# Performance work log

Measured on AMD Instinct MI355X. Metric: run time of the kernel, lower is better.

## Reference

```python
import jax, jax.numpy as jnp
import numpy as np

DIM_Q = 512
DIM_K = 512
DIM_V = 512
NUM_HEADS = 8
B, NQ, NK = 4, 2048, 2048


def _linear_init(key, d_in, d_out):
    kw, kb = jax.random.split(key)
    bound = 1.0 / np.sqrt(d_in)
    W = jax.random.uniform(kw, (d_in, d_out), minval=-bound, maxval=bound, dtype=jnp.float32)
    b = jax.random.uniform(kb, (d_out,), minval=-bound, maxval=bound, dtype=jnp.float32)
    return W, b


def setup_inputs() -> dict:
    key = jax.random.key(0)
    ks = jax.random.split(key, 6)
    Q = jax.random.normal(ks[0], (B, NQ, DIM_Q), dtype=jnp.float32)
    K = jax.random.normal(ks[1], (B, NK, DIM_K), dtype=jnp.float32)
    Wq, bq = _linear_init(ks[2], DIM_Q, DIM_V)
    Wk, bk = _linear_init(ks[3], DIM_K, DIM_V)
    Wv, bv = _linear_init(ks[4], DIM_K, DIM_V)
    Wo, bo = _linear_init(ks[5], DIM_V, DIM_V)
    ln0_g = jnp.ones((DIM_V,), jnp.float32)
    ln0_b = jnp.zeros((DIM_V,), jnp.float32)
    ln1_g = jnp.ones((DIM_V,), jnp.float32)
    ln1_b = jnp.zeros((DIM_V,), jnp.float32)
    return {"Q": Q, "K": K, "Wq": Wq, "bq": bq, "Wk": Wk, "bk": bk,
            "Wv": Wv, "bv": bv, "Wo": Wo, "bo": bo,
            "ln0_g": ln0_g, "ln0_b": ln0_b, "ln1_g": ln1_g, "ln1_b": ln1_b}


def _layer_norm(x, g, b, eps=1e-5):
    mu = jnp.mean(x, axis=-1, keepdims=True)
    var = jnp.mean(jnp.square(x - mu), axis=-1, keepdims=True)
    return (x - mu) * jax.lax.rsqrt(var + eps) * g + b


def reference(Q, K, Wq, bq, Wk, bk, Wv, bv, Wo, bo, ln0_g, ln0_b, ln1_g, ln1_b):
    h = NUM_HEADS
    dh = DIM_V // h
    q = Q @ Wq + bq                      # [B, NQ, DIM_V]
    k = K @ Wk + bk                      # [B, NK, DIM_V]
    v = K @ Wv + bv                      # [B, NK, DIM_V]
    qh = q.reshape(B, NQ, h, dh)
    kh = k.reshape(B, NK, h, dh)
    vh = v.reshape(B, NK, h, dh)
    # NOTE: faithful to original — scale by sqrt(dim_V), not sqrt(head_dim)
    scores = jnp.einsum('bqhd,bkhd->bhqk', qh, kh) / jnp.sqrt(jnp.float32(DIM_V))
    A = jax.nn.softmax(scores, axis=-1)  # [B, h, NQ, NK]
    o = jnp.einsum('bhqk,bkhd->bqhd', A, vh) + qh
    H = o.reshape(B, NQ, DIM_V)          # residual with projected Q
    H = _layer_norm(H, ln0_g, ln0_b)
    H = H + jax.nn.relu(H @ Wo + bo)
    H = _layer_norm(H, ln1_g, ln1_b)
    return H
```

## Files before the change

### kernel.cpp

```cpp
#include <hip/hip_runtime.h>

typedef float f32x4 __attribute__((ext_vector_type(4)));
typedef float f32x16 __attribute__((ext_vector_type(16)));
typedef __bf16 bf16x8 __attribute__((ext_vector_type(8)));
typedef unsigned short u16;
typedef u16 u16x8 __attribute__((ext_vector_type(8)));
typedef u16 u16x4 __attribute__((ext_vector_type(4)));

#define SCALE2F (0.044194173824159216f * 1.4426950408889634f)
#define UNSCALE (1.0f / SCALE2F)

__device__ __forceinline__ u16 f2bf(float x){ return __builtin_bit_cast(u16, (__bf16)x); }
__device__ __forceinline__ float bf2f(u16 h){ unsigned u = ((unsigned)h) << 16; return __builtin_bit_cast(float, u); }
__device__ __forceinline__ int swz(int r, int byteInRow){ return (r*128 + byteInRow) ^ ((r & 7) << 4); }
__device__ __forceinline__ void gload16(const void* g, void* l) {
  __builtin_amdgcn_global_load_lds(
      (const __attribute__((address_space(1))) void*)g,
      (__attribute__((address_space(3))) void*)l, 16, 0, 0);
}

#define MFMA(a,b,c)   __builtin_amdgcn_mfma_f32_16x16x32_bf16((a),(b),(c),0,0,0)
#define MFMA32(a,b,c) __builtin_amdgcn_mfma_f32_32x32x16_bf16((a),(b),(c),0,0,0)

__global__ __launch_bounds__(256) void wprep_k(
    const float* __restrict__ W0, const float* __restrict__ W1,
    const float* __restrict__ W2, const float* __restrict__ W3,
    u16* __restrict__ wt)
{
  __shared__ float tile[64][68];
  const float* Ws[4] = {W0, W1, W2, W3};
  const float* W = Ws[blockIdx.z];
  const float sc = (blockIdx.z == 0) ? SCALE2F : 1.0f;
  u16* out = wt + (size_t)blockIdx.z * 512 * 512;
  int k0 = blockIdx.x * 64, n0 = blockIdx.y * 64;
  int t = threadIdx.x;
  #pragma unroll
  for (int i = 0; i < 2; ++i) {
    int c = t + i*256; int r = c >> 3, k8 = c & 7;
    const float* src = W + (size_t)(k0 + r)*512 + n0 + k8*8;
    *(f32x4*)&tile[r][k8*8]     = *(const f32x4*)src;
    *(f32x4*)&tile[r][k8*8 + 4] = *(const f32x4*)(src + 4);
  }
  __syncthreads();
  #pragma unroll
  for (int i = 0; i < 2; ++i) {
    int c = t + i*256; int r = c >> 3, k8 = c & 7;
    u16x8 h;
    #pragma unroll
    for (int j = 0; j < 8; ++j) h[j] = f2bf(tile[k8*8 + j][r] * sc);
    *(u16x8*)(out + (size_t)(n0 + r)*512 + k0 + k8*8) = h;
  }
}

__global__ __launch_bounds__(512) void proj3_k(
    const float* __restrict__ Qin, const float* __restrict__ Kin,
    const u16* __restrict__ wt,
    const float* __restrict__ bq, const float* __restrict__ bk, const float* __restrict__ bv,
    u16* __restrict__ qbuf, u16* __restrict__ kbuf, u16* __restrict__ vt)
{
  __shared__ __align__(16) u16 lA[2][64*64];
  __shared__ __align__(16) u16 lB[2][128*64];
  int z = blockIdx.z;
  const float* A    = (z == 0) ? Qin : Kin;
  const u16*   Bt   = wt + (size_t)z * 262144;
  const float* bias = (z == 0) ? bq : (z == 1) ? bk : bv;
  const float bscale = (z == 0) ? SCALE2F : 1.0f;
  int row0 = blockIdx.x * 64, col0 = blockIdx.y * 128;
  int t = threadIdx.x, lane = t & 63, wid = t >> 6;
  int wr = wid >> 2, wc = wid & 3;
  int l15 = lane & 15, lg = lane >> 4;
  int ar = t >> 3, ak8 = t & 7;
  int br = t >> 3;
  int bsrc = (((t & 7) << 4) ^ ((br & 7) << 4)) >> 1;
  const float* Arow = A + (size_t)row0 * 512;
  const u16*   Brow = Bt + (size_t)col0 * 512;

  f32x4 acc[2][2] = {};

  #pragma unroll
  for (int i = 0; i < 2; ++i)
    gload16(Brow + (size_t)(br + i*64)*512 + bsrc, (char*)lB[0] + i*8192 + t*16);
  {
    const float* src = Arow + (size_t)ar*512 + ak8*8;
    f32x4 x0 = *(const f32x4*)src;
    f32x4 x1 = *(const f32x4*)(src + 4);
    u16x8 h;
    #pragma unroll
    for (int j = 0; j < 4; ++j) { h[j] = f2bf(x0[j]); h[j+4] = f2bf(x1[j]); }
    *(u16x8*)((char*)lA[0] + swz(ar, ak8*16)) = h;
  }
  __syncthreads();

  int cur = 0;
  for (int k0 = 0; k0 < 512; k0 += 64) {
    bool pf = (k0 + 64 < 512);
    f32x4 px0, px1;
    if (pf) {
      #pragma unroll
      for (int i = 0; i < 2; ++i)
        gload16(Brow + (size_t)(br + i*64)*512 + k0 + 64 + bsrc, (char*)lB[cur^1] + i*8192 + t*16);
      const float* src = Arow + (size_t)ar*512 + k0 + 64 + ak8*8;
      px0 = *(const f32x4*)src;
      px1 = *(const f32x4*)(src + 4);
    }
    const char* lAc = (const char*)lA[cur];
    const char* lBc = (const char*)lB[cur];
    #pragma unroll
    for (int ks = 0; ks < 2; ++ks) {
      bf16x8 af[2], bfv[2];
      #pragma unroll
      for (int m = 0; m < 2; ++m)
        af[m] = *(const bf16x8*)(lAc + swz(wr*32 + m*16 + l15, ks*64 + lg*16));
      #pragma unroll
      for (int n = 0; n < 2; ++n)
        bfv[n] = *(const bf16x8*)(lBc + swz(wc*32 + n*16 + l15, ks*64 + lg*16));
      #pragma unroll
      for (int m = 0; m < 2; ++m)
        #pragma unroll
        for (int n = 0; n < 2; ++n)
          acc[m][n] = MFMA(af[m], bfv[n], acc[m][n]);
    }
    if (pf) {
      u16x8 h;
      #pragma unroll
      for (int j = 0; j < 4; ++j) { h[j] = f2bf(px0[j]); h[j+4] = f2bf(px1[j]); }
      *(u16x8*)((char*)lA[cur^1] + swz(ar, ak8*16)) = h;
    }
    __syncthreads();
    cur ^= 1;
  }

  if (z < 2) {
    u16* out = z ? kbuf : qbuf;
    #pragma unroll
    for (int m = 0; m < 2; ++m) {
      int rowg = row0 + wr*32 + m*16 + lg*4;
      #pragma unroll
      for (int n = 0; n < 2; ++n) {
        int colg = col0 + wc*32 + n*16 + l15;
        float bvv = bias[colg] * bscale;
        #pragma unroll
        for (int r = 0; r < 4; ++r)
          out[(size_t)(rowg + r)*512 + colg] = f2bf(acc[m][n][r] + bvv);
      }
    }
  } else {
    #pragma unroll
    for (int m = 0; m < 2; ++m) {
      int rowg = row0 + wr*32 + m*16 + lg*4;
      int b = rowg >> 11, ntok = rowg & 2047;
      #pragma unroll
      for (int n = 0; n < 2; ++n) {
        int colg = col0 + wc*32 + n*16 + l15;
        float bvv = bias[colg];
        u16x4 hv;
        #pragma unroll
        for (int r = 0; r < 4; ++r) hv[r] = f2bf(acc[m][n][r] + bvv);
        *(u16x4*)(vt + ((size_t)b*512 + colg)*2048 + ntok) = hv;
      }
    }
  }
}

__global__ __launch_bounds__(512) void gemmo_k(
    const u16* __restrict__ A, const u16* __restrict__ Bt,
    const float* __restrict__ bias, float* __restrict__ outf,
    const u16* __restrict__ resid)
{
  __shared__ __align__(16) u16 lA[2][64*64];
  __shared__ __align__(16) u16 lB[2][128*64];
  int row0 = blockIdx.x * 64, col0 = blockIdx.y * 128;
  int t = threadIdx.x, lane = t & 63, wid = t >> 6;
  int wr = wid >> 2, wc = wid & 3;
  int l15 = lane & 15, lg = lane >> 4;
  int ar = t >> 3;
  int asrc = (((t & 7) << 4) ^ ((ar & 7) << 4)) >> 1;
  const u16* Arow = A + (size_t)row0 * 512;
  const u16* Brow = Bt + (size_t)col0 * 512;
  f32x4 acc[2][2] = {};

  gload16(Arow + (size_t)ar*512 + asrc, (char*)lA[0] + t*16);
  #pragma unroll
  for (int i = 0; i < 2; ++i)
    gload16(Brow + (size_t)(ar + i*64)*512 + asrc, (char*)lB[0] + i*8192 + t*16);
  __syncthreads();

  int cur = 0;
  for (int k0 = 0; k0 < 512; k0 += 64) {
    if (k0 + 64 < 512) {
      gload16(Arow + (size_t)ar*512 + k0 + 64 + asrc, (char*)lA[cur^1] + t*16);
      #pragma unroll
      for (int i = 0; i < 2; ++i)
        gload16(Brow + (size_t)(ar + i*64)*512 + k0 + 64 + asrc, (char*)lB[cur^1] + i*8192 + t*16);
    }
    const char* lAc = (const char*)lA[cur];
    const char* lBc = (const char*)lB[cur];
    #pragma unroll
    for (int ks = 0; ks < 2; ++ks) {
      bf16x8 af[2], bfv[2];
      #pragma unroll
      for (int m = 0; m < 2; ++m)
        af[m] = *(const bf16x8*)(lAc + swz(wr*32 + m*16 + l15, ks*64 + lg*16));
      #pragma unroll
      for (int n = 0; n < 2; ++n)
        bfv[n] = *(const bf16x8*)(lBc + swz(wc*32 + n*16 + l15, ks*64 + lg*16));
      #pragma unroll
      for (int m = 0; m < 2; ++m)
        #pragma unroll
        for (int n = 0; n < 2; ++n)
          acc[m][n] = MFMA(af[m], bfv[n], acc[m][n]);
    }
    __syncthreads();
    cur ^= 1;
  }
  #pragma unroll
  for (int m = 0; m < 2; ++m) {
    int rowg = row0 + wr*32 + m*16 + lg*4;
    #pragma unroll
    for (int n = 0; n < 2; ++n) {
      int colg = col0 + wc*32 + n*16 + l15;
      float bvv = bias[colg];
      #pragma unroll
      for (int r = 0; r < 4; ++r) {
        size_t idx = (size_t)(rowg + r)*512 + colg;
        outf[idx] = bf2f(resid[idx]) + fmaxf(acc[m][n][r] + bvv, 0.0f);
      }
    }
  }
}

__global__ __launch_bounds__(512, 4) void attn_k(
    const u16* __restrict__ qb, const u16* __restrict__ kb,
    const u16* __restrict__ vt, float* __restrict__ opart, float* __restrict__ psb)
{
  __shared__ __align__(16) u16 lK[2][64*64];
  __shared__ __align__(16) u16 lV[2][64*64];
  __shared__ __align__(16) u16 pl[8][32][72];

  int t = threadIdx.x, lane = t & 63, wid = t >> 6;
  int bh = blockIdx.y;
  int b = bh >> 3, h = bh & 7;
  int zkv = blockIdx.z;
  int kvbeg = zkv * 1024, kvend = kvbeg + 1024;
  int q0 = blockIdx.x * 256 + wid * 32;
  int l31 = lane & 31, hi = lane >> 5;

  const u16* kbase = kb + ((size_t)b*2048)*512 + h*64;
  const u16* vbase = vt + ((size_t)b*512 + h*64)*2048;

  int sr = t >> 3;
  int ssrc = (((t & 7) << 4) ^ ((sr & 7) << 4)) >> 1;

  bf16x8 aq[4];
  {
    const u16* qp = qb + ((size_t)(b*2048 + q0 + l31))*512 + h*64 + hi*8;
    #pragma unroll
    for (int ks = 0; ks < 4; ++ks) aq[ks] = *(const bf16x8*)(qp + ks*16);
  }

  f32x16 acco[2] = {};
  float ps = 0.0f;

  gload16(kbase + (size_t)(kvbeg + sr)*512 + ssrc, (char*)lK[0] + t*16);
  gload16(vbase + (size_t)sr*2048 + kvbeg + ssrc, (char*)lV[0] + t*16);
  __syncthreads();

  int cur = 0;
  for (int t0 = kvbeg; t0 < kvend; t0 += 64) {
    if (t0 + 64 < kvend) {
      gload16(kbase + (size_t)(t0 + 64 + sr)*512 + ssrc, (char*)lK[cur^1] + t*16);
      gload16(vbase + (size_t)sr*2048 + t0 + 64 + ssrc, (char*)lV[cur^1] + t*16);
    }
    const char* lKc = (const char*)lK[cur];
    const char* lVc = (const char*)lV[cur];
    #pragma unroll
    for (int n = 0; n < 2; ++n) {
      f32x16 s = {};
      #pragma unroll
      for (int ks = 0; ks < 4; ++ks) {
        bf16x8 kf = *(const bf16x8*)(lKc + swz(n*32 + l31, ks*32 + hi*16));
        s = MFMA32(kf, aq[ks], s);
      }
      #pragma unroll
      for (int rq = 0; rq < 4; ++rq) {
        u16x4 hp;
        #pragma unroll
        for (int e = 0; e < 4; ++e) {
          float p = __builtin_amdgcn_exp2f(s[rq*4 + e]);
          ps += p;
          hp[e] = f2bf(p);
        }
        *(u16x4*)&pl[wid][l31][n*32 + rq*8 + hi*4] = hp;
      }
    }
    bf16x8 pf[4];
    #pragma unroll
    for (int ks = 0; ks < 4; ++ks)
      pf[ks] = *(const bf16x8*)&pl[wid][l31][ks*16 + hi*8];
    #pragma unroll
    for (int m = 0; m < 2; ++m)
      #pragma unroll
      for (int ks = 0; ks < 4; ++ks) {
        bf16x8 vf = *(const bf16x8*)(lVc + swz(m*32 + l31, ks*32 + hi*16));
        acco[m] = MFMA32(vf, pf[ks], acco[m]);
      }
    __syncthreads();
    cur ^= 1;
  }
  ps += __shfl_xor(ps, 32, 64);
  float* obase = opart + (((size_t)zkv*4 + b)*2048 + q0 + l31)*512 + h*64;
  #pragma unroll
  for (int m = 0; m < 2; ++m)
    #pragma unroll
    for (int rq = 0; rq < 4; ++rq) {
      f32x4 ov;
      #pragma unroll
      for (int e = 0; e < 4; ++e) ov[e] = acco[m][rq*4 + e];
      *(f32x4*)(obase + m*32 + rq*8 + hi*4) = ov;
    }
  if (hi == 0)
    psb[((size_t)zkv*32 + bh)*2048 + q0 + l31] = ps;
}

__global__ __launch_bounds__(256) void ln0c_k(
    const float* __restrict__ opart, const float* __restrict__ psb,
    const u16* __restrict__ qb, const float* __restrict__ gam,
    const float* __restrict__ bet, u16* __restrict__ yh)
{
  int t = threadIdx.x, lane = t & 63, w = t >> 6;
  size_t row = (size_t)blockIdx.x * 4 + w;
  int b = (int)(row >> 11), q = (int)(row & 2047);
  int head = lane >> 3;
  float sa = psb[((size_t)b*8 + head)*2048 + q] +
             psb[((size_t)32 + b*8 + head)*2048 + q];
  float inv = 1.0f / sa;
  const float* xa = opart + row*512 + lane*8;
  const float* xb = xa + (size_t)8192*512;
  f32x4 a0 = *(const f32x4*)xa,      a1 = *(const f32x4*)(xa + 4);
  f32x4 b0v = *(const f32x4*)xb,     b1v = *(const f32x4*)(xb + 4);
  u16x8 qr = *(const u16x8*)(qb + row*512 + lane*8);
  f32x4 v0, v1;
  #pragma unroll
  for (int j = 0; j < 4; ++j) {
    v0[j] = (a0[j] + b0v[j])*inv + bf2f(qr[j])*UNSCALE;
    v1[j] = (a1[j] + b1v[j])*inv + bf2f(qr[j+4])*UNSCALE;
  }
  float s = 0.0f, ss = 0.0f;
  #pragma unroll
  for (int j = 0; j < 4; ++j) {
    s += v0[j] + v1[j];
    ss += v0[j]*v0[j] + v1[j]*v1[j];
  }
  #pragma unroll
  for (int m = 1; m < 64; m <<= 1) { s += __shfl_xor(s, m, 64); ss += __shfl_xor(ss, m, 64); }
  float mu = s * (1.0f/512.0f);
  float var = ss * (1.0f/512.0f) - mu*mu;
  float rs = rsqrtf(var + 1e-5f);
  const float* gp = gam + lane*8;
  const float* bp = bet + lane*8;
  f32x4 g0 = *(const f32x4*)gp, g1 = *(const f32x4*)(gp + 4);
  f32x4 be0 = *(const f32x4*)bp, be1 = *(const f32x4*)(bp + 4);
  u16x8 hv;
  #pragma unroll
  for (int j = 0; j < 4; ++j) {
    hv[j]   = f2bf((v0[j] - mu)*rs*g0[j] + be0[j]);
    hv[j+4] = f2bf((v1[j] - mu)*rs*g1[j] + be1[j]);
  }
  *(u16x8*)(yh + row*512 + lane*8) = hv;
}

__global__ __launch_bounds__(256) void ln_k(
    const float* __restrict__ x, const float* __restrict__ gam,
    const float* __restrict__ bet, float* __restrict__ y)
{
  int t = threadIdx.x, lane = t & 63, w = t >> 6;
  size_t row = (size_t)blockIdx.x * 4 + w;
  const float* xp = x + row*512 + lane*8;
  f32x4 v0 = *(const f32x4*)xp;
  f32x4 v1 = *(const f32x4*)(xp + 4);
  float s = 0.0f, ss = 0.0f;
  #pragma unroll
  for (int j = 0; j < 4; ++j) {
    s += v0[j] + v1[j];
    ss += v0[j]*v0[j] + v1[j]*v1[j];
  }
  #pragma unroll
  for (int m = 1; m < 64; m <<= 1) { s += __shfl_xor(s, m, 64); ss += __shfl_xor(ss, m, 64); }
  float mu = s * (1.0f/512.0f);
  float var = ss * (1.0f/512.0f) - mu*mu;
  float rs = rsqrtf(var + 1e-5f);
  const float* gp = gam + lane*8;
  const float* bp = bet + lane*8;
  f32x4 g0 = *(const f32x4*)gp, g1 = *(const f32x4*)(gp + 4);
  f32x4 b0 = *(const f32x4*)bp, b1 = *(const f32x4*)(bp + 4);
  f32x4 o0, o1;
  #pragma unroll
  for (int j = 0; j < 4; ++j) {
    o0[j] = (v0[j] - mu)*rs*g0[j] + b0[j];
    o1[j] = (v1[j] - mu)*rs*g1[j] + b1[j];
  }
  float* yp = y + row*512 + lane*8;
  *(f32x4*)yp = o0;
  *(f32x4*)(yp + 4) = o1;
}

extern "C" void kernel_launch(void* const* d_in, const int* in_sizes, int n_in,
                              void* d_out, int out_size, void* d_ws, size_t ws_size,
                              hipStream_t stream)
{
  const float* Q   = (const float*)d_in[0];
  const float* K   = (const float*)d_in[1];
  const float* Wq  = (const float*)d_in[2];
  const float* bq  = (const float*)d_in[3];
  const float* Wk  = (const float*)d_in[4];
  const float* bk  = (const float*)d_in[5];
  const float* Wv  = (const float*)d_in[6];
  const float* bv  = (const float*)d_in[7];
  const float* Wo  = (const float*)d_in[8];
  const float* bo  = (const float*)d_in[9];
  const float* g0  = (const float*)d_in[10];
  const float* b0  = (const float*)d_in[11];
  const float* g1  = (const float*)d_in[12];
  const float* b1  = (const float*)d_in[13];

  char* ws = (char*)d_ws;
  u16*   wt    = (u16*)(ws + 0);
  u16*   qbuf  = (u16*)(ws + (2u<<20));
  u16*   kbuf  = (u16*)(ws + (10u<<20));
  u16*   vt    = (u16*)(ws + (18u<<20));
  float* opart = (float*)(ws + (26u<<20));
  float* psb   = (float*)(ws + (58u<<20));
  u16*   Hbuf  = (u16*)(ws + (10u<<20));
  float* Gbuf  = (float*)(ws + (26u<<20));

  wprep_k<<<dim3(8, 8, 4), 256, 0, stream>>>(Wq, Wk, Wv, Wo, wt);
  proj3_k<<<dim3(128, 4, 3), 512, 0, stream>>>(Q, K, wt, bq, bk, bv, qbuf, kbuf, vt);
  attn_k<<<dim3(8, 32, 2), 512, 0, stream>>>(qbuf, kbuf, vt, opart, psb);
  ln0c_k<<<2048, 256, 0, stream>>>(opart, psb, qbuf, g0, b0, Hbuf);
  gemmo_k<<<dim3(128, 4), 512, 0, stream>>>(Hbuf, wt + 3*262144, bo, Gbuf, Hbuf);
  ln_k<<<2048, 256, 0, stream>>>(Gbuf, g1, b1, (float*)d_out);
}
```

Measured before the change: 105.6 us.

## Register-resident P via permlane swap, two Q tiles per wave, bf16 intermediates

The attention kernel now gives each wave 64 query rows, handled as two 32-row tiles that share every K/V LDS fragment, and drops to 256 threads per block. It builds the bf16 probability operand in registers using v_cvt_pk_bf16_f32 and v_permlane32_swap, which removes the per-wave LDS round trip for P. The partial attention outputs and the gemmo output are stored as bf16 instead of fp32, roughly halving traffic into ln0c_k and ln_k. The trade-off is higher register pressure in attn_k and some accuracy loss from rounding the intermediates to bf16.

```diff
diff --git a/kernel.cpp b/kernel.cpp
--- a/kernel.cpp
+++ b/kernel.cpp
@@ -4,8 +4,10 @@
 typedef float f32x16 __attribute__((ext_vector_type(16)));
 typedef __bf16 bf16x8 __attribute__((ext_vector_type(8)));
 typedef unsigned short u16;
+typedef unsigned int u32;
 typedef u16 u16x8 __attribute__((ext_vector_type(8)));
 typedef u16 u16x4 __attribute__((ext_vector_type(4)));
+typedef u32 u32x4 __attribute__((ext_vector_type(4)));
 
 #define SCALE2F (0.044194173824159216f * 1.4426950408889634f)
 #define UNSCALE (1.0f / SCALE2F)
@@ -17,6 +19,14 @@
   __builtin_amdgcn_global_load_lds(
       (const __attribute__((address_space(1))) void*)g,
       (__attribute__((address_space(3))) void*)l, 16, 0, 0);
+}
+__device__ __forceinline__ u32 cvtpk(float lo, float hi_) {
+  u32 r;
+  asm("v_cvt_pk_bf16_f32 %0, %1, %2" : "=v"(r) : "v"(lo), "v"(hi_));
+  return r;
+}
+__device__ __forceinline__ void swap32(u32 &a, u32 &b) {
+  asm("v_permlane32_swap_b32 %0, %1" : "+v"(a), "+v"(b));
 }
 
 #define MFMA(a,b,c)   __builtin_amdgcn_mfma_f32_16x16x32_bf16((a),(b),(c),0,0,0)
@@ -164,7 +174,7 @@
 
 __global__ __launch_bounds__(512) void gemmo_k(
     const u16* __restrict__ A, const u16* __restrict__ Bt,
-    const float* __restrict__ bias, float* __restrict__ outf,
+    const float* __restrict__ bias, u16* __restrict__ outb,
     const u16* __restrict__ resid)
 {
   __shared__ __align__(16) u16 lA[2][64*64];
@@ -223,107 +233,126 @@
       #pragma unroll
       for (int r = 0; r < 4; ++r) {
         size_t idx = (size_t)(rowg + r)*512 + colg;
-        outf[idx] = bf2f(resid[idx]) + fmaxf(acc[m][n][r] + bvv, 0.0f);
-      }
-    }
-  }
-}
-
-__global__ __launch_bounds__(512, 4) void attn_k(
+        outb[idx] = f2bf(bf2f(resid[idx]) + fmaxf(acc[m][n][r] + bvv, 0.0f));
+      }
+    }
+  }
+}
+
+__device__ __forceinline__ void mk_pb(const f32x16& s, float& ps, bf16x8& f0, bf16x8& f1) {
+  float p[16];
+  #pragma unroll
+  for (int r = 0; r < 16; ++r) { p[r] = __builtin_amdgcn_exp2f(s[r]); ps += p[r]; }
+  u32 a0 = cvtpk(p[0],  p[1]),  b0 = cvtpk(p[4],  p[5]);
+  u32 a1 = cvtpk(p[2],  p[3]),  b1 = cvtpk(p[6],  p[7]);
+  swap32(a0, b0); swap32(a1, b1);
+  u32 a2 = cvtpk(p[8],  p[9]),  b2 = cvtpk(p[12], p[13]);
+  u32 a3 = cvtpk(p[10], p[11]), b3 = cvtpk(p[14], p[15]);
+  swap32(a2, b2); swap32(a3, b3);
+  u32x4 w0 = {a0, a1, b0, b1};
+  u32x4 w1 = {a2, a3, b2, b3};
+  f0 = __builtin_bit_cast(bf16x8, w0);
+  f1 = __builtin_bit_cast(bf16x8, w1);
+}
+
+__global__ __launch_bounds__(256, 2) void attn_k(
     const u16* __restrict__ qb, const u16* __restrict__ kb,
-    const u16* __restrict__ vt, float* __restrict__ opart, float* __restrict__ psb)
+    const u16* __restrict__ vt, u16* __restrict__ opart, float* __restrict__ psb)
 {
   __shared__ __align__(16) u16 lK[2][64*64];
   __shared__ __align__(16) u16 lV[2][64*64];
-  __shared__ __align__(16) u16 pl[8][32][72];
 
   int t = threadIdx.x, lane = t & 63, wid = t >> 6;
-  int bh = blockIdx.y;
-  int b = bh >> 3, h = bh & 7;
+  int bh = blockIdx.y, b = bh >> 3, h = bh & 7;
   int zkv = blockIdx.z;
-  int kvbeg = zkv * 1024, kvend = kvbeg + 1024;
-  int q0 = blockIdx.x * 256 + wid * 32;
+  int kvbeg = zkv * 1024;
+  int q0 = blockIdx.x * 256 + wid * 64;
   int l31 = lane & 31, hi = lane >> 5;
 
   const u16* kbase = kb + ((size_t)b*2048)*512 + h*64;
   const u16* vbase = vt + ((size_t)b*512 + h*64)*2048;
 
   int sr = t >> 3;
-  int ssrc = (((t & 7) << 4) ^ ((sr & 7) << 4)) >> 1;
-
-  bf16x8 aq[4];
+  int ssrc = ((t & 7) ^ (sr & 7)) << 3;
+
+#define STAGE(buf, kvoff)                                                              \
+  gload16(kbase + (size_t)((kvoff) + sr)*512 + ssrc,       (char*)lK[buf] + t*16);     \
+  gload16(kbase + (size_t)((kvoff) + 32 + sr)*512 + ssrc,  (char*)lK[buf] + 4096 + t*16); \
+  gload16(vbase + (size_t)sr*2048 + (kvoff) + ssrc,        (char*)lV[buf] + t*16);     \
+  gload16(vbase + (size_t)(32 + sr)*2048 + (kvoff) + ssrc, (char*)lV[buf] + 4096 + t*16);
+
+  bf16x8 aqA[4], aqB[4];
   {
-    const u16* qp = qb + ((size_t)(b*2048 + q0 + l31))*512 + h*64 + hi*8;
-    #pragma unroll
-    for (int ks = 0; ks < 4; ++ks) aq[ks] = *(const bf16x8*)(qp + ks*16);
-  }
-
-  f32x16 acco[2] = {};
-  float ps = 0.0f;
-
-  gload16(kbase + (size_t)(kvbeg + sr)*512 + ssrc, (char*)lK[0] + t*16);
-  gload16(vbase + (size_t)sr*2048 + kvbeg + ssrc, (char*)lV[0] + t*16);
+    const u16* qpA = qb + ((size_t)(b*2048 + q0 + l31))*512 + h*64 + hi*8;
+    const u16* qpB = qpA + (size_t)32*512;
+    #pragma unroll
+    for (int ks = 0; ks < 4; ++ks) {
+      aqA[ks] = *(const bf16x8*)(qpA + ks*16);
+      aqB[ks] = *(const bf16x8*)(qpB + ks*16);
+    }
+  }
+
+  f32x16 accA[2] = {}, accB[2] = {};
+  float psA = 0.0f, psB = 0.0f;
+
+  STAGE(0, kvbeg);
   __syncthreads();
 
   int cur = 0;
-  for (int t0 = kvbeg; t0 < kvend; t0 += 64) {
-    if (t0 + 64 < kvend) {
-      gload16(kbase + (size_t)(t0 + 64 + sr)*512 + ssrc, (char*)lK[cur^1] + t*16);
-      gload16(vbase + (size_t)sr*2048 + t0 + 64 + ssrc, (char*)lV[cur^1] + t*16);
-    }
+  for (int t0 = kvbeg; t0 < kvbeg + 1024; t0 += 64) {
+    if (t0 + 64 < kvbeg + 1024) { STAGE(cur^1, t0 + 64); }
     const char* lKc = (const char*)lK[cur];
     const char* lVc = (const char*)lV[cur];
+    bf16x8 pbA[4], pbB[4];
     #pragma unroll
     for (int n = 0; n < 2; ++n) {
-      f32x16 s = {};
+      f32x16 s0 = {}, s1 = {};
       #pragma unroll
       for (int ks = 0; ks < 4; ++ks) {
         bf16x8 kf = *(const bf16x8*)(lKc + swz(n*32 + l31, ks*32 + hi*16));
-        s = MFMA32(kf, aq[ks], s);
-      }
-      #pragma unroll
-      for (int rq = 0; rq < 4; ++rq) {
-        u16x4 hp;
-        #pragma unroll
-        for (int e = 0; e < 4; ++e) {
-          float p = __builtin_amdgcn_exp2f(s[rq*4 + e]);
-          ps += p;
-          hp[e] = f2bf(p);
-        }
-        *(u16x4*)&pl[wid][l31][n*32 + rq*8 + hi*4] = hp;
-      }
-    }
-    bf16x8 pf[4];
-    #pragma unroll
-    for (int ks = 0; ks < 4; ++ks)
-      pf[ks] = *(const bf16x8*)&pl[wid][l31][ks*16 + hi*8];
+        s0 = MFMA32(kf, aqA[ks], s0);
+        s1 = MFMA32(kf, aqB[ks], s1);
+      }
+      mk_pb(s0, psA, pbA[2*n], pbA[2*n+1]);
+      mk_pb(s1, psB, pbB[2*n], pbB[2*n+1]);
+    }
     #pragma unroll
     for (int m = 0; m < 2; ++m)
       #pragma unroll
       for (int ks = 0; ks < 4; ++ks) {
         bf16x8 vf = *(const bf16x8*)(lVc + swz(m*32 + l31, ks*32 + hi*16));
-        acco[m] = MFMA32(vf, pf[ks], acco[m]);
+        accA[m] = MFMA32(vf, pbA[ks], accA[m]);
+        accB[m] = MFMA32(vf, pbB[ks], accB[m]);
       }
     __syncthreads();
     cur ^= 1;
   }
-  ps += __shfl_xor(ps, 32, 64);
-  float* obase = opart + (((size_t)zkv*4 + b)*2048 + q0 + l31)*512 + h*64;
+#undef STAGE
+  psA += __shfl_xor(psA, 32, 64);
+  psB += __shfl_xor(psB, 32, 64);
+  u16* oA = opart + (((size_t)zkv*4 + b)*2048 + q0 + l31)*512 + h*64;
+  u16* oB = oA + (size_t)32*512;
   #pragma unroll
   for (int m = 0; m < 2; ++m)
     #pragma unroll
     for (int rq = 0; rq < 4; ++rq) {
-      f32x4 ov;
-      #pragma unroll
-      for (int e = 0; e < 4; ++e) ov[e] = acco[m][rq*4 + e];
-      *(f32x4*)(obase + m*32 + rq*8 + hi*4) = ov;
-    }
-  if (hi == 0)
-    psb[((size_t)zkv*32 + bh)*2048 + q0 + l31] = ps;
+      u16x4 hA, hB;
+      #pragma unroll
+      for (int e = 0; e < 4; ++e) {
+        hA[e] = f2bf(accA[m][rq*4 + e]);
+        hB[e] = f2bf(accB[m][rq*4 + e]);
+      }
+      *(u16x4*)(oA + m*32 + rq*8 + hi*4) = hA;
+      *(u16x4*)(oB + m*32 + rq*8 + hi*4) = hB;
+    }
+  if (hi == 0) {
+    psb[((size_t)zkv*32 + bh)*2048 + q0 + l31]      = psA;
+    psb[((size_t)zkv*32 + bh)*2048 + q0 + 32 + l31] = psB;
+  }
 }
 
 __global__ __launch_bounds__(256) void ln0c_k(
-    const float* __restrict__ opart, const float* __restrict__ psb,
+    const u16* __restrict__ opart, const float* __restrict__ psb,
     const u16* __restrict__ qb, const float* __restrict__ gam,
     const float* __restrict__ bet, u16* __restrict__ yh)
 {
@@ -334,23 +363,18 @@
   float sa = psb[((size_t)b*8 + head)*2048 + q] +
              psb[((size_t)32 + b*8 + head)*2048 + q];
   float inv = 1.0f / sa;
-  const float* xa = opart + row*512 + lane*8;
-  const float* xb = xa + (size_t)8192*512;
-  f32x4 a0 = *(const f32x4*)xa,      a1 = *(const f32x4*)(xa + 4);
-  f32x4 b0v = *(const f32x4*)xb,     b1v = *(const f32x4*)(xb + 4);
-  u16x8 qr = *(const u16x8*)(qb + row*512 + lane*8);
-  f32x4 v0, v1;
-  #pragma unroll
-  for (int j = 0; j < 4; ++j) {
-    v0[j] = (a0[j] + b0v[j])*inv + bf2f(qr[j])*UNSCALE;
-    v1[j] = (a1[j] + b1v[j])*inv + bf2f(qr[j+4])*UNSCALE;
-  }
+  const u16* xa = opart + row*512 + lane*8;
+  const u16* xb = xa + (size_t)8192*512;
+  u16x8 av  = *(const u16x8*)xa;
+  u16x8 bv8 = *(const u16x8*)xb;
+  u16x8 qr  = *(const u16x8*)(qb + row*512 + lane*8);
+  float v[8];
+  #pragma unroll
+  for (int j = 0; j < 8; ++j)
+    v[j] = (bf2f(av[j]) + bf2f(bv8[j]))*inv + bf2f(qr[j])*UNSCALE;
   float s = 0.0f, ss = 0.0f;
   #pragma unroll
-  for (int j = 0; j < 4; ++j) {
-    s += v0[j] + v1[j];
-    ss += v0[j]*v0[j] + v1[j]*v1[j];
-  }
+  for (int j = 0; j < 8; ++j) { s += v[j]; ss += v[j]*v[j]; }
   #pragma unroll
   for (int m = 1; m < 64; m <<= 1) { s += __shfl_xor(s, m, 64); ss += __shfl_xor(ss, m, 64); }
   float mu = s * (1.0f/512.0f);
@@ -363,27 +387,25 @@
   u16x8 hv;
   #pragma unroll
   for (int j = 0; j < 4; ++j) {
-    hv[j]   = f2bf((v0[j] - mu)*rs*g0[j] + be0[j]);
-    hv[j+4] = f2bf((v1[j] - mu)*rs*g1[j] + be1[j]);
+    hv[j]   = f2bf((v[j]   - mu)*rs*g0[j] + be0[j]);
+    hv[j+4] = f2bf((v[j+4] - mu)*rs*g1[j] + be1[j]);
   }
   *(u16x8*)(yh + row*512 + lane*8) = hv;
 }
 
 __global__ __launch_bounds__(256) void ln_k(
-    const float* __restrict__ x, const float* __restrict__ gam,
+    const u16* __restrict__ x, const float* __restrict__ gam,
     const float* __restrict__ bet, float* __restrict__ y)
 {
   int t = threadIdx.x, lane = t & 63, w = t >> 6;
   size_t row = (size_t)blockIdx.x * 4 + w;
-  const float* xp = x + row*512 + lane*8;
-  f32x4 v0 = *(const f32x4*)xp;
-  f32x4 v1 = *(const f32x4*)(xp + 4);
+  u16x8 xv = *(const u16x8*)(x + row*512 + lane*8);
+  float v[8];
+  #pragma unroll
+  for (int j = 0; j < 8; ++j) v[j] = bf2f(xv[j]);
   float s = 0.0f, ss = 0.0f;
   #pragma unroll
-  for (int j = 0; j < 4; ++j) {
-    s += v0[j] + v1[j];
-    ss += v0[j]*v0[j] + v1[j]*v1[j];
-  }
+  for (int j = 0; j < 8; ++j) { s += v[j]; ss += v[j]*v[j]; }
   #pragma unroll
   for (int m = 1; m < 64; m <<= 1) { s += __shfl_xor(s, m, 64); ss += __shfl_xor(ss, m, 64); }
   float mu = s * (1.0f/512.0f);
@@ -396,8 +418,8 @@
   f32x4 o0, o1;
   #pragma unroll
   for (int j = 0; j < 4; ++j) {
-    o0[j] = (v0[j] - mu)*rs*g0[j] + b0[j];
-    o1[j] = (v1[j] - mu)*rs*g1[j] + b1[j];
+    o0[j] = (v[j]   - mu)*rs*g0[j] + b0[j];
+    o1[j] = (v[j+4] - mu)*rs*g1[j] + b1[j];
   }
   float* yp = y + row*512 + lane*8;
   *(f32x4*)yp = o0;
@@ -428,15 +450,15 @@
   u16*   qbuf  = (u16*)(ws + (2u<<20));
   u16*   kbuf  = (u16*)(ws + (10u<<20));
   u16*   vt    = (u16*)(ws + (18u<<20));
-  float* opart = (float*)(ws + (26u<<20));
+  u16*   opart = (u16*)(ws + (26u<<20));
+  u16*   Gb    = (u16*)(ws + (44u<<20));
   float* psb   = (float*)(ws + (58u<<20));
   u16*   Hbuf  = (u16*)(ws + (10u<<20));
-  float* Gbuf  = (float*)(ws + (26u<<20));
 
   wprep_k<<<dim3(8, 8, 4), 256, 0, stream>>>(Wq, Wk, Wv, Wo, wt);
   proj3_k<<<dim3(128, 4, 3), 512, 0, stream>>>(Q, K, wt, bq, bk, bv, qbuf, kbuf, vt);
-  attn_k<<<dim3(8, 32, 2), 512, 0, stream>>>(qbuf, kbuf, vt, opart, psb);
+  attn_k<<<dim3(8, 32, 2), 256, 0, stream>>>(qbuf, kbuf, vt, opart, psb);
   ln0c_k<<<2048, 256, 0, stream>>>(opart, psb, qbuf, g0, b0, Hbuf);
-  gemmo_k<<<dim3(128, 4), 512, 0, stream>>>(Hbuf, wt + 3*262144, bo, Gbuf, Hbuf);
-  ln_k<<<2048, 256, 0, stream>>>(Gbuf, g1, b1, (float*)d_out);
-}
+  gemmo_k<<<dim3(128, 4), 512, 0, stream>>>(Hbuf, wt + 3*262144, bo, Gb, Hbuf);
+  ln_k<<<2048, 256, 0, stream>>>(Gb, g1, b1, (float*)d_out);
+}
```

Result: faster. 98.89 us (-6.4%).
